# Kernel tuning notes

Hardware: AMD Instinct MI355X
Metric: run time of the kernel (lower is better)

The kernel has to match this reference:

```python
import jax, jax.numpy as jnp
import numpy as np

B, IN_SIZE, OUT_SIZE, N_QUBITS, DEPTH = 4096, 512, 256, 12, 3
C64 = jnp.complex64
BN_EPS = 1e-5


def setup_inputs() -> dict:
    key = jax.random.key(0)
    ks = jax.random.split(key, 6)
    x = jax.random.normal(ks[0], (B, IN_SIZE), jnp.float32)
    enc_w = jax.random.normal(ks[1], (N_QUBITS, IN_SIZE), jnp.float32) / np.sqrt(IN_SIZE)
    enc_b = jnp.zeros((N_QUBITS,), jnp.float32)
    rot_params = jax.random.normal(ks[2], (DEPTH, N_QUBITS, 3), jnp.float32) * 0.1
    ent_params = jax.random.normal(ks[3], (DEPTH, N_QUBITS - 1), jnp.float32) * 0.1
    dec_w = jax.random.normal(ks[4], (OUT_SIZE, N_QUBITS), jnp.float32) / np.sqrt(N_QUBITS)
    dec_b = jnp.zeros((OUT_SIZE,), jnp.float32)
    return {
        'x': x, 'enc_w': enc_w, 'enc_b': enc_b,
        'rot_params': rot_params, 'ent_params': ent_params,
        'dec_w': dec_w, 'dec_b': dec_b,
        'bn1_gamma': jnp.ones((N_QUBITS,), jnp.float32),
        'bn1_beta': jnp.zeros((N_QUBITS,), jnp.float32),
        'bn2_gamma': jnp.ones((OUT_SIZE,), jnp.float32),
        'bn2_beta': jnp.zeros((OUT_SIZE,), jnp.float32),
    }


def _m2(a, b, c, d):
    return jnp.stack([jnp.stack([a, b]), jnp.stack([c, d])]).astype(C64)


def _rx(t):
    c = jnp.cos(t / 2).astype(C64)
    s = jnp.sin(t / 2).astype(C64)
    return _m2(c, -1j * s, -1j * s, c)


def _ry(t):
    c = jnp.cos(t / 2)
    s = jnp.sin(t / 2)
    return _m2(c, -s, s, c)


def _rz(p):
    z = jnp.zeros((), C64)
    return _m2(jnp.exp(-1j * p / 2), z, z, jnp.exp(1j * p / 2))


def _apply_1q(state, U, q):
    # state: [B, 2^n]; apply 2x2 U on qubit q (qubit 0 = most significant axis)
    b = state.shape[0]
    s = state.reshape(b, 2 ** q, 2, -1)
    s = jnp.einsum('ij,bkjl->bkil', U, s)
    return s.reshape(b, -1)


def _apply_cry(state, theta, q):
    # controlled-Ry: control qubit q, target qubit q+1 (adjacent)
    b = state.shape[0]
    R = _ry(theta)
    st = state.reshape(b, 2 ** q, 2, 2, -1)
    s0 = st[:, :, 0]
    s1 = jnp.einsum('ij,bkjl->bkil', R, st[:, :, 1])
    return jnp.stack([s0, s1], axis=2).reshape(b, -1)


def _batchnorm(x, g, b):
    # BatchNorm1d in training mode: biased batch stats
    m = x.mean(0)
    v = x.var(0)
    return g * (x - m) / jnp.sqrt(v + BN_EPS) + b


def _quantum_forward(encoded, rot_params, ent_params):
    # Batched statevector simulation of the per-sample circuit.
    b, n = encoded.shape
    depth = rot_params.shape[0]
    # amplitude encoding: normalize, theta = 2*arcsin(clip(|a|,0,1)), P(pi) if a<0
    norm = jnp.linalg.norm(encoded, axis=1, keepdims=True)
    a = jnp.where(norm > 0, encoded / jnp.maximum(norm, 1e-30), encoded)
    amp = jnp.clip(jnp.abs(a), 0.0, 1.0)              # sin(theta/2)
    cos_h = jnp.sqrt(jnp.maximum(1.0 - amp * amp, 0.0))  # cos(theta/2)
    sgn = jnp.where(a < 0, -1.0, 1.0)                  # P(pi) flips sign of |1> amp
    qvec = jnp.stack([cos_h, sgn * amp], axis=-1).astype(C64)  # [B, n, 2]
    # product state via successive outer products (loop over fixed n qubits)
    state = jnp.ones((b, 1), C64)
    for q in range(n):
        state = (state[:, :, None] * qvec[:, q, None, :]).reshape(b, -1)
    # parameterized circuit
    for l in range(depth):
        for q in range(n):
            U = _rz(rot_params[l, q, 2]) @ _ry(rot_params[l, q, 1]) @ _rx(rot_params[l, q, 0])
            state = _apply_1q(state, U, q)
        for q in range(n - 1):
            state = _apply_cry(state, ent_params[l, q], q)
    # per-qubit P(|1>) measurement probabilities
    idx = jnp.arange(2 ** n)
    bits = ((idx[:, None] >> (n - 1 - jnp.arange(n))) & 1).astype(jnp.float32)  # [2^n, n]
    probs = (jnp.abs(state) ** 2).astype(jnp.float32) @ bits  # [B, n]
    return probs


def reference(x, enc_w, enc_b, rot_params, ent_params, dec_w, dec_b,
              bn1_gamma, bn1_beta, bn2_gamma, bn2_beta):
    encoded = x @ enc_w.T + enc_b
    encoded = jnp.tanh(_batchnorm(encoded, bn1_gamma, bn1_beta))
    probs = _quantum_forward(encoded, rot_params, ent_params)
    out = probs @ dec_w.T + dec_b
    return _batchnorm(out, bn2_gamma, bn2_beta)
```

## Files before the change

kernel.cpp:

```cpp
#include <hip/hip_runtime.h>

#define BATCH   4096
#define IN_SZ   512
#define NQ      12
#define OUT_SZ  256
#define DEPTH   3
#define NST     4096
#define BN_EPS  1e-5f

#define OFF_ENC    0
#define OFF_BN1M   49152
#define OFF_BN1R   49168
#define OFF_GU     49184
#define OFF_GC     49472
#define OFF_PROBS  49568
#define OFF_PMEAN  98720
#define OFF_COV    98736
#define OFF_RSTD   98880

typedef float v2f __attribute__((ext_vector_type(2)));
typedef float v4f __attribute__((ext_vector_type(4)));
#define SW2(a) __builtin_shufflevector(a, a, 1, 0)

__global__ void k_encode(const float* __restrict__ x, const float* __restrict__ w,
                         const float* __restrict__ bvec,
                         const float* __restrict__ rot, const float* __restrict__ ent,
                         float* __restrict__ enc, float* __restrict__ gU, float* __restrict__ gC) {
    if (blockIdx.x == 1024) {
        int t = threadIdx.x;
        if (t < DEPTH * NQ) {
            float ax = rot[t * 3 + 0] * 0.5f;
            float ay = rot[t * 3 + 1] * 0.5f;
            float az = rot[t * 3 + 2] * 0.5f;
            float cx = cosf(ax), sx = sinf(ax);
            float cy = cosf(ay), sy = sinf(ay);
            float cz = cosf(az), sz = sinf(az);
            float m00r =  cy * cx, m00i =  sy * sx;
            float m01r = -sy * cx, m01i = -cy * sx;
            float m10r =  sy * cx, m10i = -cy * sx;
            float m11r =  cy * cx, m11i = -sy * sx;
            float* o = gU + t * 8;
            o[0] = cz * m00r + sz * m00i;  o[1] = cz * m00i - sz * m00r;
            o[2] = cz * m01r + sz * m01i;  o[3] = cz * m01i - sz * m01r;
            o[4] = cz * m10r - sz * m10i;  o[5] = cz * m10i + sz * m10r;
            o[6] = cz * m11r - sz * m11i;  o[7] = cz * m11i + sz * m11r;
        }
        if (t >= 64 && t - 64 < DEPTH * (NQ - 1)) {
            int i = t - 64;
            float th = ent[i] * 0.5f;
            gC[i * 2 + 0] = cosf(th);
            gC[i * 2 + 1] = sinf(th);
        }
        return;
    }
    int t = threadIdx.x;
    int wv = t >> 6, lane = t & 63;
    int row = blockIdx.x * 4 + wv;
    const float4* xr = (const float4*)(x + row * IN_SZ) + lane * 2;
    float4 xa = xr[0], xb = xr[1];
    float acc[NQ];
    #pragma unroll
    for (int q = 0; q < NQ; q++) {
        const float4* wr = (const float4*)(w + q * IN_SZ) + lane * 2;
        float4 wa = wr[0], wb = wr[1];
        float d = xa.x*wa.x + xa.y*wa.y + xa.z*wa.z + xa.w*wa.w
                + xb.x*wb.x + xb.y*wb.y + xb.z*wb.z + xb.w*wb.w;
        #pragma unroll
        for (int o = 32; o > 0; o >>= 1) d += __shfl_down(d, o, 64);
        acc[q] = d;
    }
    if (lane == 0) {
        float* er = enc + row * NQ;
        #pragma unroll
        for (int q = 0; q < NQ; q++) er[q] = acc[q] + bvec[q];
    }
}

__device__ float blockAllSum(float v, float* scr) {
    #pragma unroll
    for (int o = 32; o > 0; o >>= 1) v += __shfl_down(v, o, 64);
    int lane = threadIdx.x & 63, w = threadIdx.x >> 6;
    __syncthreads();
    if (lane == 0) scr[w] = v;
    __syncthreads();
    return scr[0] + scr[1] + scr[2] + scr[3];
}

__global__ void k_bnstats(const float* __restrict__ xm, float* __restrict__ mo,
                          float* __restrict__ ro) {
    __shared__ float scr[32];
    int j = blockIdx.x, t = threadIdx.x;
    float s = 0.f, s2 = 0.f;
    for (int b = t; b < BATCH; b += 1024) {
        float v = xm[b * NQ + j];
        s += v; s2 += v * v;
    }
    #pragma unroll
    for (int o = 32; o > 0; o >>= 1) { s += __shfl_down(s, o, 64); s2 += __shfl_down(s2, o, 64); }
    int lane = t & 63, w = t >> 6;
    if (lane == 0) { scr[w] = s; scr[16 + w] = s2; }
    __syncthreads();
    if (t == 0) {
        float S = 0.f, S2 = 0.f;
        #pragma unroll
        for (int i = 0; i < 16; i++) { S += scr[i]; S2 += scr[16 + i]; }
        float mean = S / (float)BATCH;
        float var  = S2 / (float)BATCH - mean * mean;
        mo[j] = mean;
        ro[j] = 1.f / sqrtf(var + BN_EPS);
    }
}

#define SLA2(j) ((T << 4) | ((((j) ^ ((T >> 1) & 7))) << 1))
#define SLB(m)  (((T & 0xF0) << 4) | ((m) << 4) | ((T & 15) ^ ((m) & 14)))
#define SLC(m)  (((m) << 8) | (T ^ ((((T >> 5) & 7)) << 1)))

#define LDA(j, Ra, Rb) { v4f t_ = *(const v4f*)(xch + SLA2(j));                 \
    Ra = __builtin_shufflevector(t_, t_, 0, 1);                                 \
    Rb = __builtin_shufflevector(t_, t_, 2, 3); }
#define STA(j, Ra, Rb) { v4f t_ = __builtin_shufflevector(Ra, Rb, 0, 1, 2, 3);  \
    *(v4f*)(xch + SLA2(j)) = t_; }

#define LOADA do { LDA(0,s0,s1) LDA(1,s2,s3) LDA(2,s4,s5) LDA(3,s6,s7)          \
    LDA(4,s8,s9) LDA(5,s10,s11) LDA(6,s12,s13) LDA(7,s14,s15) } while (0)
#define STORA do { STA(0,s0,s1) STA(1,s2,s3) STA(2,s4,s5) STA(3,s6,s7)          \
    STA(4,s8,s9) STA(5,s10,s11) STA(6,s12,s13) STA(7,s14,s15) } while (0)

#define LOADW(SL) do {                                                          \
    s0=xch[SL(0)];  s1=xch[SL(1)];  s2=xch[SL(2)];  s3=xch[SL(3)];              \
    s4=xch[SL(4)];  s5=xch[SL(5)];  s6=xch[SL(6)];  s7=xch[SL(7)];              \
    s8=xch[SL(8)];  s9=xch[SL(9)];  s10=xch[SL(10)]; s11=xch[SL(11)];           \
    s12=xch[SL(12)]; s13=xch[SL(13)]; s14=xch[SL(14)]; s15=xch[SL(15)]; } while (0)
#define STORW(SL) do {                                                          \
    xch[SL(0)]=s0;  xch[SL(1)]=s1;  xch[SL(2)]=s2;  xch[SL(3)]=s3;              \
    xch[SL(4)]=s4;  xch[SL(5)]=s5;  xch[SL(6)]=s6;  xch[SL(7)]=s7;              \
    xch[SL(8)]=s8;  xch[SL(9)]=s9;  xch[SL(10)]=s10; xch[SL(11)]=s11;           \
    xch[SL(12)]=s12; xch[SL(13)]=s13; xch[SL(14)]=s14; xch[SL(15)]=s15; } while (0)

#define U_LOADP(uptr) const float* u_ = (uptr);                                  \
    v2f c00r = {u_[0], u_[0]}, c00i = {-u_[1], u_[1]};                           \
    v2f c01r = {u_[2], u_[2]}, c01i = {-u_[3], u_[3]};                           \
    v2f c10r = {u_[4], u_[4]}, c10i = {-u_[5], u_[5]};                           \
    v2f c11r = {u_[6], u_[6]}, c11i = {-u_[7], u_[7]};

#define U_PAIRP(A, B) { v2f a0 = A, a1 = B, a0s = SW2(a0), a1s = SW2(a1);        \
    A = a0*c00r + a0s*c00i + a1*c01r + a1s*c01i;                                 \
    B = a0*c10r + a0s*c10i + a1*c11r + a1s*c11i; }

#define APPLY_U_K3(uptr) do { U_LOADP(uptr)                                      \
    U_PAIRP(s0,s8) U_PAIRP(s1,s9) U_PAIRP(s2,s10) U_PAIRP(s3,s11)                \
    U_PAIRP(s4,s12) U_PAIRP(s5,s13) U_PAIRP(s6,s14) U_PAIRP(s7,s15) } while (0)
#define APPLY_U_K2(uptr) do { U_LOADP(uptr)                                      \
    U_PAIRP(s0,s4) U_PAIRP(s1,s5) U_PAIRP(s2,s6) U_PAIRP(s3,s7)                  \
    U_PAIRP(s8,s12) U_PAIRP(s9,s13) U_PAIRP(s10,s14) U_PAIRP(s11,s15) } while (0)
#define APPLY_U_K1(uptr) do { U_LOADP(uptr)                                      \
    U_PAIRP(s0,s2) U_PAIRP(s1,s3) U_PAIRP(s4,s6) U_PAIRP(s5,s7)                  \
    U_PAIRP(s8,s10) U_PAIRP(s9,s11) U_PAIRP(s12,s14) U_PAIRP(s13,s15) } while (0)
#define APPLY_U_K0(uptr) do { U_LOADP(uptr)                                      \
    U_PAIRP(s0,s1) U_PAIRP(s2,s3) U_PAIRP(s4,s5) U_PAIRP(s6,s7)                  \
    U_PAIRP(s8,s9) U_PAIRP(s10,s11) U_PAIRP(s12,s13) U_PAIRP(s14,s15) } while (0)

#define RY_PAIRP(A, B) { v2f a0 = A, a1 = B;                                     \
    A = a0*cc2 - a1*ss2;  B = a0*ss2 + a1*cc2; }

#define CRY_32(cc, ss) do { v2f cc2 = {(cc),(cc)}, ss2 = {(ss),(ss)};            \
    RY_PAIRP(s8,s12) RY_PAIRP(s9,s13) RY_PAIRP(s10,s14) RY_PAIRP(s11,s15) } while (0)
#define CRY_21(cc, ss) do { v2f cc2 = {(cc),(cc)}, ss2 = {(ss),(ss)};            \
    RY_PAIRP(s4,s6) RY_PAIRP(s5,s7) RY_PAIRP(s12,s14) RY_PAIRP(s13,s15) } while (0)
#define CRY_10(cc, ss) do { v2f cc2 = {(cc),(cc)}, ss2 = {(ss),(ss)};            \
    RY_PAIRP(s2,s3) RY_PAIRP(s6,s7) RY_PAIRP(s10,s11) RY_PAIRP(s14,s15) } while (0)
#define RYALL_K3(cc, ss) do { v2f cc2 = {(cc),(cc)}, ss2 = {(ss),(ss)};          \
    RY_PAIRP(s0,s8) RY_PAIRP(s1,s9) RY_PAIRP(s2,s10) RY_PAIRP(s3,s11)            \
    RY_PAIRP(s4,s12) RY_PAIRP(s5,s13) RY_PAIRP(s6,s14) RY_PAIRP(s7,s15) } while (0)

#define INITJ(SR, j) { SR.x = f * (((j)&8)?qs8:qc8) * (((j)&4)?qs9:qc9)          \
    * (((j)&2)?qs10:qc10) * (((j)&1)?qs11:qc11); SR.y = 0.f; }
#define PRJ(S) ((S).x*(S).x + (S).y*(S).y)
#define WREDUCE(v) { v += __shfl_down(v,32,64); v += __shfl_down(v,16,64);       \
    v += __shfl_down(v,8,64); v += __shfl_down(v,4,64);                          \
    v += __shfl_down(v,2,64); v += __shfl_down(v,1,64); }

#define MKQ(i) float qc##i, qs##i; {                                             \
    float h_ = h##i;                                                             \
    float a_ = nz ? h_ * rinv : h_;                                              \
    float amp_ = fminf(fabsf(a_), 1.f);                                          \
    qc##i = sqrtf(fmaxf(1.f - amp_ * amp_, 0.f));                                \
    qs##i = (a_ < 0.f) ? -amp_ : amp_; }

__launch_bounds__(256)
__global__ void k_quantum(const float* __restrict__ enc,
                          const float* __restrict__ bn1m, const float* __restrict__ bn1r,
                          const float* __restrict__ g1, const float* __restrict__ b1,
                          const float* __restrict__ gU, const float* __restrict__ gC,
                          float* __restrict__ probs) {
    __shared__ __align__(16) v2f xch[NST];

    int T = threadIdx.x, b = blockIdx.x;

    const float* er = enc + b * NQ;
    float h0  = tanhf(g1[0]  * (er[0]  - bn1m[0])  * bn1r[0]  + b1[0]);
    float h1  = tanhf(g1[1]  * (er[1]  - bn1m[1])  * bn1r[1]  + b1[1]);
    float h2  = tanhf(g1[2]  * (er[2]  - bn1m[2])  * bn1r[2]  + b1[2]);
    float h3  = tanhf(g1[3]  * (er[3]  - bn1m[3])  * bn1r[3]  + b1[3]);
    float h4  = tanhf(g1[4]  * (er[4]  - bn1m[4])  * bn1r[4]  + b1[4]);
    float h5  = tanhf(g1[5]  * (er[5]  - bn1m[5])  * bn1r[5]  + b1[5]);
    float h6  = tanhf(g1[6]  * (er[6]  - bn1m[6])  * bn1r[6]  + b1[6]);
    float h7  = tanhf(g1[7]  * (er[7]  - bn1m[7])  * bn1r[7]  + b1[7]);
    float h8  = tanhf(g1[8]  * (er[8]  - bn1m[8])  * bn1r[8]  + b1[8]);
    float h9  = tanhf(g1[9]  * (er[9]  - bn1m[9])  * bn1r[9]  + b1[9]);
    float h10 = tanhf(g1[10] * (er[10] - bn1m[10]) * bn1r[10] + b1[10]);
    float h11 = tanhf(g1[11] * (er[11] - bn1m[11]) * bn1r[11] + b1[11]);
    float n2 = h0*h0+h1*h1+h2*h2+h3*h3+h4*h4+h5*h5+h6*h6+h7*h7
             + h8*h8+h9*h9+h10*h10+h11*h11;
    float norm = sqrtf(n2);
    bool  nz   = norm > 0.f;
    float rinv = 1.f / fmaxf(norm, 1e-30f);
    MKQ(0) MKQ(1) MKQ(2) MKQ(3) MKQ(4) MKQ(5) MKQ(6) MKQ(7)
    MKQ(8) MKQ(9) MKQ(10) MKQ(11)

    v2f s0, s1, s2, s3, s4, s5, s6, s7, s8, s9, s10, s11, s12, s13, s14, s15;

    {
        float f = ((T>>7)&1 ? qs0 : qc0) * ((T>>6)&1 ? qs1 : qc1)
                * ((T>>5)&1 ? qs2 : qc2) * ((T>>4)&1 ? qs3 : qc3)
                * ((T>>3)&1 ? qs4 : qc4) * ((T>>2)&1 ? qs5 : qc5)
                * ((T>>1)&1 ? qs6 : qc6) * ((T>>0)&1 ? qs7 : qc7);
        INITJ(s0,0)  INITJ(s1,1)  INITJ(s2,2)  INITJ(s3,3)
        INITJ(s4,4)  INITJ(s5,5)  INITJ(s6,6)  INITJ(s7,7)
        INITJ(s8,8)  INITJ(s9,9)  INITJ(s10,10) INITJ(s11,11)
        INITJ(s12,12) INITJ(s13,13) INITJ(s14,14) INITJ(s15,15)
        APPLY_U_K3(gU + 8 * 8);
        APPLY_U_K2(gU + 9 * 8);
        APPLY_U_K1(gU + 10 * 8);
        APPLY_U_K0(gU + 11 * 8);
        STORA;
        __builtin_amdgcn_wave_barrier();
    }

    #pragma unroll 1
    for (int l = 0; l < DEPTH; l++) {
        const float* UL = gU + l * 96;
        const float* CL = gC + l * 22;
        LOADW(SLB);
        APPLY_U_K3(UL + 4 * 8);
        APPLY_U_K2(UL + 5 * 8);
        APPLY_U_K1(UL + 6 * 8);
        APPLY_U_K0(UL + 7 * 8);
        STORW(SLB);
        __syncthreads();
        LOADW(SLC);
        APPLY_U_K3(UL + 0 * 8);
        APPLY_U_K2(UL + 1 * 8);
        APPLY_U_K1(UL + 2 * 8);
        APPLY_U_K0(UL + 3 * 8);
        CRY_32(CL[0], CL[1]);
        CRY_21(CL[2], CL[3]);
        CRY_10(CL[4], CL[5]);
        STORW(SLC);
        __syncthreads();
        LOADW(SLB);
        if (T & 16) RYALL_K3(CL[6], CL[7]);
        CRY_32(CL[8], CL[9]);
        CRY_21(CL[10], CL[11]);
        CRY_10(CL[12], CL[13]);
        STORW(SLB);
        __builtin_amdgcn_wave_barrier();
        LOADA;
        if (T & 1) RYALL_K3(CL[14], CL[15]);
        CRY_32(CL[16], CL[17]);
        CRY_21(CL[18], CL[19]);
        CRY_10(CL[20], CL[21]);
        if (l < DEPTH - 1) {
            const float* UN = gU + (l + 1) * 96;
            APPLY_U_K3(UN + 8 * 8);
            APPLY_U_K2(UN + 9 * 8);
            APPLY_U_K1(UN + 10 * 8);
            APPLY_U_K0(UN + 11 * 8);
            STORA;
            __builtin_amdgcn_wave_barrier();
        }
    }

    float p0 = PRJ(s0),  p1 = PRJ(s1),  p2 = PRJ(s2),  p3 = PRJ(s3);
    float p4 = PRJ(s4),  p5 = PRJ(s5),  p6 = PRJ(s6),  p7 = PRJ(s7);
    float p8 = PRJ(s8),  p9 = PRJ(s9),  p10 = PRJ(s10), p11 = PRJ(s11);
    float p12 = PRJ(s12), p13 = PRJ(s13), p14 = PRJ(s14), p15 = PRJ(s15);
    float tot = p0+p1+p2+p3+p4+p5+p6+p7+p8+p9+p10+p11+p12+p13+p14+p15;
    float r8  = p8+p9+p10+p11+p12+p13+p14+p15;
    float r9  = p4+p5+p6+p7+p12+p13+p14+p15;
    float r10 = p2+p3+p6+p7+p10+p11+p14+p15;
    float r11 = p1+p3+p5+p7+p9+p11+p13+p15;
    float r0 = (T & 128) ? tot : 0.f;
    float r1 = (T & 64)  ? tot : 0.f;
    float r2 = (T & 32)  ? tot : 0.f;
    float r3 = (T & 16)  ? tot : 0.f;
    float r4 = (T & 8)   ? tot : 0.f;
    float r5 = (T & 4)   ? tot : 0.f;
    float r6 = (T & 2)   ? tot : 0.f;
    float r7 = (T & 1)   ? tot : 0.f;

    WREDUCE(r0) WREDUCE(r1) WREDUCE(r2) WREDUCE(r3) WREDUCE(r4) WREDUCE(r5)
    WREDUCE(r6) WREDUCE(r7) WREDUCE(r8) WREDUCE(r9) WREDUCE(r10) WREDUCE(r11)

    __syncthreads();
    float* red = (float*)xch;
    int lane = T & 63, w = T >> 6;
    if (lane == 0) {
        float* rr = red + w * NQ;
        rr[0]=r0; rr[1]=r1; rr[2]=r2; rr[3]=r3; rr[4]=r4; rr[5]=r5;
        rr[6]=r6; rr[7]=r7; rr[8]=r8; rr[9]=r9; rr[10]=r10; rr[11]=r11;
    }
    __syncthreads();
    if (T < NQ) probs[b * NQ + T] = red[T] + red[NQ + T] + red[2 * NQ + T] + red[3 * NQ + T];
}

__global__ void k_pcov(const float* __restrict__ probs, float* __restrict__ pmean,
                       float* __restrict__ cov) {
    __shared__ float scr[8];
    int blk = blockIdx.x;
    int q = blk / NQ, q2 = blk % NQ;
    int t = threadIdx.x;
    float sx = 0.f, sy = 0.f, sxy = 0.f;
    for (int b = t; b < BATCH; b += 256) {
        float xv = probs[b * NQ + q];
        float yv = probs[b * NQ + q2];
        sx += xv; sy += yv; sxy += xv * yv;
    }
    float SX  = blockAllSum(sx,  scr);
    float SY  = blockAllSum(sy,  scr);
    float SXY = blockAllSum(sxy, scr);
    if (t == 0) {
        float mx = SX / (float)BATCH, my = SY / (float)BATCH;
        cov[blk] = SXY / (float)BATCH - mx * my;
        if (q == q2) pmean[q] = mx;
    }
}

__global__ void k_rstd(const float* __restrict__ cov, const float* __restrict__ dw,
                       float* __restrict__ rstd) {
    __shared__ float cv[NQ * NQ];
    int t = threadIdx.x;
    if (t < NQ * NQ) cv[t] = cov[t];
    __syncthreads();
    float w[NQ];
    #pragma unroll
    for (int q = 0; q < NQ; q++) w[q] = dw[t * NQ + q];
    float var = 0.f;
    #pragma unroll
    for (int q = 0; q < NQ; q++) {
        float a = 0.f;
        #pragma unroll
        for (int q2 = 0; q2 < NQ; q2++) a += cv[q * NQ + q2] * w[q2];
        var += w[q] * a;
    }
    rstd[t] = 1.f / sqrtf(var + BN_EPS);
}

__global__ void k_final(const float* __restrict__ probs, const float* __restrict__ pmean,
                        const float* __restrict__ rstd, const float* __restrict__ dw,
                        const float* __restrict__ g2, const float* __restrict__ b2,
                        float* __restrict__ out) {
    __shared__ float cp[2][NQ];
    int b0 = blockIdx.x * 2;
    int t = threadIdx.x;
    int half = t >> 8, j = t & 255;
    if (t < NQ)                      cp[0][t]       = probs[b0 * NQ + t]        - pmean[t];
    else if (t >= 256 && t < 256+NQ) cp[1][t - 256] = probs[(b0+1) * NQ + t-256] - pmean[t - 256];
    __syncthreads();
    float acc = 0.f;
    #pragma unroll
    for (int q = 0; q < NQ; q++) acc += cp[half][q] * dw[j * NQ + q];
    out[(b0 + half) * OUT_SZ + j] = acc * rstd[j] * g2[j] + b2[j];
}

extern "C" void kernel_launch(void* const* d_in, const int* in_sizes, int n_in,
                              void* d_out, int out_size, void* d_ws, size_t ws_size,
                              hipStream_t stream) {
    const float* x     = (const float*)d_in[0];
    const float* enc_w = (const float*)d_in[1];
    const float* enc_b = (const float*)d_in[2];
    const float* rot   = (const float*)d_in[3];
    const float* ent   = (const float*)d_in[4];
    const float* dec_w = (const float*)d_in[5];
    const float* g1    = (const float*)d_in[7];
    const float* b1    = (const float*)d_in[8];
    const float* g2    = (const float*)d_in[9];
    const float* b2    = (const float*)d_in[10];

    float* ws    = (float*)d_ws;
    float* enc   = ws + OFF_ENC;
    float* bn1m  = ws + OFF_BN1M;
    float* bn1r  = ws + OFF_BN1R;
    float* gU    = ws + OFF_GU;
    float* gC    = ws + OFF_GC;
    float* prb   = ws + OFF_PROBS;
    float* pmean = ws + OFF_PMEAN;
    float* cov   = ws + OFF_COV;
    float* rstd  = ws + OFF_RSTD;

    hipLaunchKernelGGL(k_encode, dim3(1025), dim3(256), 0, stream,
                       x, enc_w, enc_b, rot, ent, enc, gU, gC);
    hipLaunchKernelGGL(k_bnstats, dim3(NQ), dim3(1024), 0, stream, enc, bn1m, bn1r);
    hipLaunchKernelGGL(k_quantum, dim3(BATCH), dim3(256), 0, stream,
                       enc, bn1m, bn1r, g1, b1, gU, gC, prb);
    hipLaunchKernelGGL(k_pcov, dim3(NQ * NQ), dim3(256), 0, stream, prb, pmean, cov);
    hipLaunchKernelGGL(k_rstd, dim3(1), dim3(OUT_SZ), 0, stream, cov, dec_w, rstd);
    hipLaunchKernelGGL(k_final, dim3(BATCH / 2), dim3(512), 0, stream,
                       prb, pmean, rstd, dec_w, g2, b2, (float*)d_out);
}
```

Measured before the change: 221.5 us.

## Reorder qubit-layout schedule to remove one block barrier per circuit layer

```diff
diff --git a/kernel.cpp b/kernel.cpp
--- a/kernel.cpp
+++ b/kernel.cpp
@@ -173,8 +173,8 @@
     RY_PAIRP(s0,s8) RY_PAIRP(s1,s9) RY_PAIRP(s2,s10) RY_PAIRP(s3,s11)            \
     RY_PAIRP(s4,s12) RY_PAIRP(s5,s13) RY_PAIRP(s6,s14) RY_PAIRP(s7,s15) } while (0)
 
-#define INITJ(SR, j) { SR.x = f * (((j)&8)?qs8:qc8) * (((j)&4)?qs9:qc9)          \
-    * (((j)&2)?qs10:qc10) * (((j)&1)?qs11:qc11); SR.y = 0.f; }
+#define INITJC(SR, j) { SR.x = f * (((j)&8)?qs0:qc0) * (((j)&4)?qs1:qc1)         \
+    * (((j)&2)?qs2:qc2) * (((j)&1)?qs3:qc3); SR.y = 0.f; }
 #define PRJ(S) ((S).x*(S).x + (S).y*(S).y)
 #define WREDUCE(v) { v += __shfl_down(v,32,64); v += __shfl_down(v,16,64);       \
     v += __shfl_down(v,8,64); v += __shfl_down(v,4,64);                          \
@@ -221,21 +221,24 @@
     v2f s0, s1, s2, s3, s4, s5, s6, s7, s8, s9, s10, s11, s12, s13, s14, s15;
 
     {
-        float f = ((T>>7)&1 ? qs0 : qc0) * ((T>>6)&1 ? qs1 : qc1)
-                * ((T>>5)&1 ? qs2 : qc2) * ((T>>4)&1 ? qs3 : qc3)
-                * ((T>>3)&1 ? qs4 : qc4) * ((T>>2)&1 ? qs5 : qc5)
-                * ((T>>1)&1 ? qs6 : qc6) * ((T>>0)&1 ? qs7 : qc7);
-        INITJ(s0,0)  INITJ(s1,1)  INITJ(s2,2)  INITJ(s3,3)
-        INITJ(s4,4)  INITJ(s5,5)  INITJ(s6,6)  INITJ(s7,7)
-        INITJ(s8,8)  INITJ(s9,9)  INITJ(s10,10) INITJ(s11,11)
-        INITJ(s12,12) INITJ(s13,13) INITJ(s14,14) INITJ(s15,15)
-        APPLY_U_K3(gU + 8 * 8);
-        APPLY_U_K2(gU + 9 * 8);
-        APPLY_U_K1(gU + 10 * 8);
-        APPLY_U_K0(gU + 11 * 8);
-        STORA;
-        __builtin_amdgcn_wave_barrier();
-    }
+        float f = ((T>>7)&1 ? qs4 : qc4) * ((T>>6)&1 ? qs5 : qc5)
+                * ((T>>5)&1 ? qs6 : qc6) * ((T>>4)&1 ? qs7 : qc7)
+                * ((T>>3)&1 ? qs8 : qc8) * ((T>>2)&1 ? qs9 : qc9)
+                * ((T>>1)&1 ? qs10 : qc10) * ((T>>0)&1 ? qs11 : qc11);
+        INITJC(s0,0)  INITJC(s1,1)  INITJC(s2,2)  INITJC(s3,3)
+        INITJC(s4,4)  INITJC(s5,5)  INITJC(s6,6)  INITJC(s7,7)
+        INITJC(s8,8)  INITJC(s9,9)  INITJC(s10,10) INITJC(s11,11)
+        INITJC(s12,12) INITJC(s13,13) INITJC(s14,14) INITJC(s15,15)
+        APPLY_U_K3(gU + 0 * 8);
+        APPLY_U_K2(gU + 1 * 8);
+        APPLY_U_K1(gU + 2 * 8);
+        APPLY_U_K0(gU + 3 * 8);
+        CRY_32(gC[0], gC[1]);
+        CRY_21(gC[2], gC[3]);
+        CRY_10(gC[4], gC[5]);
+        STORW(SLC);
+    }
+    __syncthreads();
 
     #pragma unroll 1
     for (int l = 0; l < DEPTH; l++) {
@@ -246,19 +249,6 @@
         APPLY_U_K2(UL + 5 * 8);
         APPLY_U_K1(UL + 6 * 8);
         APPLY_U_K0(UL + 7 * 8);
-        STORW(SLB);
-        __syncthreads();
-        LOADW(SLC);
-        APPLY_U_K3(UL + 0 * 8);
-        APPLY_U_K2(UL + 1 * 8);
-        APPLY_U_K1(UL + 2 * 8);
-        APPLY_U_K0(UL + 3 * 8);
-        CRY_32(CL[0], CL[1]);
-        CRY_21(CL[2], CL[3]);
-        CRY_10(CL[4], CL[5]);
-        STORW(SLC);
-        __syncthreads();
-        LOADW(SLB);
         if (T & 16) RYALL_K3(CL[6], CL[7]);
         CRY_32(CL[8], CL[9]);
         CRY_21(CL[10], CL[11]);
@@ -266,18 +256,29 @@
         STORW(SLB);
         __builtin_amdgcn_wave_barrier();
         LOADA;
+        APPLY_U_K3(UL + 8 * 8);
+        APPLY_U_K2(UL + 9 * 8);
+        APPLY_U_K1(UL + 10 * 8);
+        APPLY_U_K0(UL + 11 * 8);
         if (T & 1) RYALL_K3(CL[14], CL[15]);
         CRY_32(CL[16], CL[17]);
         CRY_21(CL[18], CL[19]);
         CRY_10(CL[20], CL[21]);
         if (l < DEPTH - 1) {
+            STORA;
+            __syncthreads();
             const float* UN = gU + (l + 1) * 96;
-            APPLY_U_K3(UN + 8 * 8);
-            APPLY_U_K2(UN + 9 * 8);
-            APPLY_U_K1(UN + 10 * 8);
-            APPLY_U_K0(UN + 11 * 8);
-            STORA;
-            __builtin_amdgcn_wave_barrier();
+            const float* CN = gC + (l + 1) * 22;
+            LOADW(SLC);
+            APPLY_U_K3(UN + 0 * 8);
+            APPLY_U_K2(UN + 1 * 8);
+            APPLY_U_K1(UN + 2 * 8);
+            APPLY_U_K0(UN + 3 * 8);
+            CRY_32(CN[0], CN[1]);
+            CRY_21(CN[2], CN[3]);
+            CRY_10(CN[4], CN[5]);
+            STORW(SLC);
+            __syncthreads();
         }
     }
 
```

Measured after the change: 216.2 us. 1.02x faster.
